# Kernel optimization log

Hardware: AMD Instinct MI355X
Metric: run time of the kernel (lower is better)

The kernel has to match this reference:

```python
import jax, jax.numpy as jnp
import numpy as np

IN_V, OUT_V, IN_E = 64, 64, 64
B, N, E = 2, 1024, 8192


def setup_inputs() -> dict:
    key = jax.random.key(0)
    ks = jax.random.split(key, 8)
    return {
        "H_v": jax.random.normal(ks[0], (B * N, IN_V), dtype=jnp.float32),
        "H_e": jax.random.normal(ks[1], (B * E, IN_E), dtype=jnp.float32),
        "adj_e": jax.random.uniform(ks[2], (B * E, E), dtype=jnp.float32),
        "adj_v": jax.random.uniform(ks[3], (B * N, N), dtype=jnp.float32),
        "T": jax.random.uniform(ks[4], (B * N, E), dtype=jnp.float32),
        "weight": jax.random.normal(ks[5], (IN_V, OUT_V), dtype=jnp.float32) * (1.0 / np.sqrt(OUT_V)),
        "p": jax.random.normal(ks[6], (1, IN_E), dtype=jnp.float32),
        "bias": jax.random.normal(ks[7], (OUT_V,), dtype=jnp.float32) * (1.0 / np.sqrt(OUT_V)),
    }


def reference(H_v, H_e, adj_e, adj_v, T, weight, p, bias):
    # node_layer=True branch of AlternateConvolution
    b = adj_v.shape[0] // adj_v.shape[1]
    n = adj_v.shape[1]
    e = adj_e.shape[1]
    H_v = H_v.reshape(b, n, -1)            # [B,N,in_v]
    H_e = H_e.reshape(b, e, -1)            # [B,E,in_e]
    adj_v = adj_v.reshape(b, n, n)         # [B,N,N]
    T = T.reshape(b, n, e)                 # [B,N,E]
    # diag_embed(H_e @ p^T) then T @ diag @ T^T == row-scale T by (H_e @ p^T) then GEMM
    scale = jnp.einsum('bef,f->be', H_e, p[0])                  # [B,E]
    multiplier1 = jnp.einsum('bne,be,bme->bnm', T, scale, T)    # [B,N,N]
    eye = jnp.eye(n, dtype=bool)
    M1 = jnp.where(eye[None, :, :], jnp.ones_like(multiplier1), multiplier1)
    adjusted_A = M1 * adj_v
    output = jnp.einsum('bnm,bmd->bnd', adjusted_A, H_v @ weight) + bias
    return output, H_e
```

## Files before the change

### kernel.cpp

```cpp
#include <hip/hip_runtime.h>

#define Bb 2
#define Nn 1024
#define Ee 8192
#define DV 64

typedef __attribute__((ext_vector_type(8))) short short8;
typedef __attribute__((ext_vector_type(8))) unsigned short ushort8;
typedef __attribute__((ext_vector_type(4))) float floatx4;

static __device__ __forceinline__ unsigned short f2bf(float f) {
    unsigned int u = __float_as_uint(f);
    unsigned int r = (u + 0x7FFFu + ((u >> 16) & 1u)) >> 16;
    return (unsigned short)r;
}
static __device__ __forceinline__ float bf2f(unsigned short u) {
    return __uint_as_float(((unsigned int)u) << 16);
}

__global__ __launch_bounds__(256) void scale_kernel(const float* __restrict__ He,
                                                    const float* __restrict__ p,
                                                    float* __restrict__ scale) {
    int wave = threadIdx.x >> 6;
    int lane = threadIdx.x & 63;
    int row = blockIdx.x * 4 + wave;
    float v = He[row * 64 + lane] * p[lane];
    #pragma unroll
    for (int off = 32; off > 0; off >>= 1) v += __shfl_xor(v, off);
    if (lane == 0) scale[row] = v;
}

__global__ __launch_bounds__(256) void cast_kernel(const float* __restrict__ T,
                                                   const float* __restrict__ scale,
                                                   unsigned short* __restrict__ Tsc,
                                                   unsigned short* __restrict__ Tpl) {
    size_t i4 = (size_t)blockIdx.x * 256 + threadIdx.x;
    size_t e0 = i4 * 4;
    int b = (int)(e0 >> 23);
    int e = (int)(e0 & 8191);
    floatx4 t = *(const floatx4*)&T[e0];
    floatx4 s = *(const floatx4*)&scale[(size_t)b * Ee + e];
    ushort4 sc, pl;
    sc.x = f2bf(t.x * s.x); sc.y = f2bf(t.y * s.y);
    sc.z = f2bf(t.z * s.z); sc.w = f2bf(t.w * s.w);
    pl.x = f2bf(t.x); pl.y = f2bf(t.y);
    pl.z = f2bf(t.z); pl.w = f2bf(t.w);
    *(ushort4*)&Tsc[e0] = sc;
    *(ushort4*)&Tpl[e0] = pl;
}

__global__ __launch_bounds__(256) void hw_kernel(const float* __restrict__ Hv,
                                                 const float* __restrict__ W,
                                                 float* __restrict__ HWo) {
    __shared__ float Ws[64 * 64];
    __shared__ float Hvs[4 * 64];
    int t = threadIdx.x;
    for (int i = t; i < 4096; i += 256) Ws[i] = W[i];
    int r0 = blockIdx.x * 4;
    Hvs[t] = Hv[(size_t)r0 * 64 + t];
    __syncthreads();
    int d = t & 63, rr = t >> 6;
    float acc = 0.f;
    #pragma unroll
    for (int c = 0; c < 64; ++c) acc += Hvs[rr * 64 + c] * Ws[c * 64 + d];
    HWo[(size_t)(r0 + rr) * 64 + d] = acc;
}

__global__ __launch_bounds__(256) void binit_kernel(const float* __restrict__ bias,
                                                    float* __restrict__ out) {
    int idx = (blockIdx.x * 256 + threadIdx.x) * 4;
    floatx4 bv = *(const floatx4*)&bias[idx & 63];
    *(floatx4*)&out[idx] = bv;
}

__global__ __launch_bounds__(256, 2) void mm_kernel(const unsigned short* __restrict__ Tsc,
                                                    const unsigned short* __restrict__ Tpl,
                                                    unsigned short* __restrict__ Ppart) {
    __shared__ __attribute__((aligned(16))) unsigned short As[128 * 64];
    __shared__ __attribute__((aligned(16))) unsigned short Bs[128 * 64];
    const int t = threadIdx.x;
    const int tile = blockIdx.x;
    const int b = blockIdx.y;
    const int s = blockIdx.z;

    int i = 0, rem = tile;
    while (rem >= 8 - i) { rem -= 8 - i; ++i; }
    const int j = i + rem;
    const int n0 = i * 128, m0 = j * 128;

    const int lane = t & 63;
    const int w = t >> 6;
    const int wr = w >> 1, wc = w & 1;
    const int quad = lane >> 4;
    const int l15 = lane & 15;
    const int l7 = l15 & 7;

    const int lr = lane >> 3;
    const int lc = (lane & 7) ^ lr;

    const int kc0 = (s * 128) / 7 * 64;
    const int kc1 = ((s + 1) * 128) / 7 * 64;

    const unsigned short* gA = Tsc + ((size_t)b * Nn + n0 + w * 32 + lr) * Ee + kc0 + lc * 8;
    const unsigned short* gB = Tpl + ((size_t)b * Nn + m0 + w * 32 + lr) * Ee + kc0 + lc * 8;
    unsigned short* lA = As + (w * 32) * 64 + lane * 8;
    unsigned short* lB = Bs + (w * 32) * 64 + lane * 8;

    floatx4 acc[4][4];
    #pragma unroll
    for (int a = 0; a < 4; ++a)
        #pragma unroll
        for (int c = 0; c < 4; ++c) acc[a][c] = (floatx4){0.f, 0.f, 0.f, 0.f};

    for (int k0 = kc0; k0 < kc1; k0 += 64) {
        #pragma unroll
        for (int u = 0; u < 4; ++u) {
            __builtin_amdgcn_global_load_lds(
                (const __attribute__((address_space(1))) unsigned int*)(gA + (size_t)u * 8 * Ee),
                (__attribute__((address_space(3))) unsigned int*)(lA + u * 8 * 64), 16, 0, 0);
            __builtin_amdgcn_global_load_lds(
                (const __attribute__((address_space(1))) unsigned int*)(gB + (size_t)u * 8 * Ee),
                (__attribute__((address_space(3))) unsigned int*)(lB + u * 8 * 64), 16, 0, 0);
        }
        gA += 64; gB += 64;
        __syncthreads();
        #pragma unroll
        for (int kk8 = 0; kk8 < 8; kk8 += 4) {
            short8 af[4], bf[4];
            #pragma unroll
            for (int a = 0; a < 4; ++a)
                af[a] = *(const short8*)&As[(wr * 64 + a * 16 + l15) * 64 + ((kk8 + quad) ^ l7) * 8];
            #pragma unroll
            for (int c = 0; c < 4; ++c)
                bf[c] = *(const short8*)&Bs[(wc * 64 + c * 16 + l15) * 64 + ((kk8 + quad) ^ l7) * 8];
            #pragma unroll
            for (int a = 0; a < 4; ++a)
                #pragma unroll
                for (int c = 0; c < 4; ++c)
                    acc[a][c] = __builtin_amdgcn_mfma_f32_16x16x32_bf16(af[a], bf[c], acc[a][c], 0, 0, 0);
        }
        __syncthreads();
    }

    unsigned short* P = Ppart + (((size_t)(b * 36 + tile)) * 7 + s) * 16384;
    #pragma unroll
    for (int a = 0; a < 4; ++a)
        #pragma unroll
        for (int c = 0; c < 4; ++c)
            #pragma unroll
            for (int v = 0; v < 4; ++v) {
                int r = wr * 64 + a * 16 + quad * 4 + v;
                int cc = wc * 64 + c * 16 + l15;
                P[r * 128 + cc] = f2bf(acc[a][c][v]);
            }
}

__global__ __launch_bounds__(256) void fuse_kernel(const unsigned short* __restrict__ Ppart,
                                                   const float* __restrict__ adj_v,
                                                   const float* __restrict__ HWo,
                                                   float* __restrict__ out) {
    __shared__ float Ls[64 * 68];
    __shared__ float Lsn[64 * 68];
    __shared__ float Lst[64 * 68];
    const int t = threadIdx.x;
    const int job = blockIdx.x;
    const int quad = blockIdx.y;
    const int b = job / 36;
    const int tile = job % 36;
    int i = 0, rem = tile;
    while (rem >= 8 - i) { rem -= 8 - i; ++i; }
    const int j = i + rem;
    const int qr = quad >> 1, qc = quad & 1;
    const int n0 = i * 128 + qr * 64;
    const int m0 = j * 128 + qc * 64;
    const unsigned short* P = Ppart + (size_t)job * 7 * 16384 + (qr * 64) * 128 + qc * 64;
    const float* AV = adj_v + (size_t)b * Nn * Nn;
    const float* HW = HWo + (size_t)b * Nn * 64;

    {
        int r = t >> 2, c0 = (t & 3) * 16;
        float sv[16];
        #pragma unroll
        for (int x = 0; x < 16; ++x) sv[x] = 0.f;
        #pragma unroll
        for (int sp = 0; sp < 7; ++sp) {
            const unsigned short* ps = P + sp * 16384 + r * 128 + c0;
            ushort8 u0 = *(const ushort8*)ps;
            ushort8 u1 = *(const ushort8*)(ps + 8);
            #pragma unroll
            for (int x = 0; x < 8; ++x) {
                sv[x] += bf2f(u0[x]);
                sv[8 + x] += bf2f(u1[x]);
            }
        }
        if (i == j && qr == qc) {
            int dcol = r - c0;
            if (dcol >= 0 && dcol < 16) sv[dcol] = 1.0f;
        }
        #pragma unroll
        for (int x4 = 0; x4 < 4; ++x4) {
            floatx4 v = (floatx4){sv[x4 * 4], sv[x4 * 4 + 1], sv[x4 * 4 + 2], sv[x4 * 4 + 3]};
            *(floatx4*)&Ls[r * 68 + c0 + x4 * 4] = v;
            floatx4 a = *(const floatx4*)&AV[(size_t)(n0 + r) * Nn + m0 + c0 + x4 * 4];
            floatx4 o = (floatx4){v.x * a.x, v.y * a.y, v.z * a.z, v.w * a.w};
            *(floatx4*)&Lsn[r * 68 + c0 + x4 * 4] = o;
        }
    }
    __syncthreads();
    if (i != j) {
        int m = t >> 2, r0 = (t & 3) * 16;
        #pragma unroll
        for (int x4 = 0; x4 < 4; ++x4) {
            floatx4 a = *(const floatx4*)&AV[(size_t)(m0 + m) * Nn + n0 + r0 + x4 * 4];
            floatx4 o;
            o.x = Ls[(r0 + x4 * 4 + 0) * 68 + m] * a.x;
            o.y = Ls[(r0 + x4 * 4 + 1) * 68 + m] * a.y;
            o.z = Ls[(r0 + x4 * 4 + 2) * 68 + m] * a.z;
            o.w = Ls[(r0 + x4 * 4 + 3) * 68 + m] * a.w;
            *(floatx4*)&Lst[m * 68 + r0 + x4 * 4] = o;
        }
    }
    __syncthreads();

    const int tr = t >> 4, tc = t & 15;
    {
        floatx4 acc[4];
        #pragma unroll
        for (int ii = 0; ii < 4; ++ii) acc[ii] = (floatx4){0.f, 0.f, 0.f, 0.f};
        #pragma unroll
        for (int k4 = 0; k4 < 64; k4 += 4) {
            floatx4 bmat[4];
            #pragma unroll
            for (int u = 0; u < 4; ++u)
                bmat[u] = *(const floatx4*)&HW[(size_t)(m0 + k4 + u) * 64 + tc * 4];
            #pragma unroll
            for (int ii = 0; ii < 4; ++ii) {
                floatx4 av = *(const floatx4*)&Lsn[(tr * 4 + ii) * 68 + k4];
                acc[ii] += av.x * bmat[0];
                acc[ii] += av.y * bmat[1];
                acc[ii] += av.z * bmat[2];
                acc[ii] += av.w * bmat[3];
            }
        }
        #pragma unroll
        for (int ii = 0; ii < 4; ++ii) {
            float* op = &out[(size_t)(b * Nn + n0 + tr * 4 + ii) * 64 + tc * 4];
            atomicAdd(op + 0, acc[ii].x);
            atomicAdd(op + 1, acc[ii].y);
            atomicAdd(op + 2, acc[ii].z);
            atomicAdd(op + 3, acc[ii].w);
        }
    }
    if (i != j) {
        floatx4 acc[4];
        #pragma unroll
        for (int ii = 0; ii < 4; ++ii) acc[ii] = (floatx4){0.f, 0.f, 0.f, 0.f};
        #pragma unroll
        for (int k4 = 0; k4 < 64; k4 += 4) {
            floatx4 bmat[4];
            #pragma unroll
            for (int u = 0; u < 4; ++u)
                bmat[u] = *(const floatx4*)&HW[(size_t)(n0 + k4 + u) * 64 + tc * 4];
            #pragma unroll
            for (int ii = 0; ii < 4; ++ii) {
                floatx4 av = *(const floatx4*)&Lst[(tr * 4 + ii) * 68 + k4];
                acc[ii] += av.x * bmat[0];
                acc[ii] += av.y * bmat[1];
                acc[ii] += av.z * bmat[2];
                acc[ii] += av.w * bmat[3];
            }
        }
        #pragma unroll
        for (int ii = 0; ii < 4; ++ii) {
            float* op = &out[(size_t)(b * Nn + m0 + tr * 4 + ii) * 64 + tc * 4];
            atomicAdd(op + 0, acc[ii].x);
            atomicAdd(op + 1, acc[ii].y);
            atomicAdd(op + 2, acc[ii].z);
            atomicAdd(op + 3, acc[ii].w);
        }
    }
}

extern "C" void kernel_launch(void* const* d_in, const int* in_sizes, int n_in,
                              void* d_out, int out_size, void* d_ws, size_t ws_size,
                              hipStream_t stream) {
    const float* H_v    = (const float*)d_in[0];
    const float* H_e    = (const float*)d_in[1];
    const float* adj_v  = (const float*)d_in[3];
    const float* T      = (const float*)d_in[4];
    const float* weight = (const float*)d_in[5];
    const float* p      = (const float*)d_in[6];
    const float* bias   = (const float*)d_in[7];
    float* out = (float*)d_out;

    char* ws = (char*)d_ws;
    float* scale          = (float*)ws;
    float* HWo            = (float*)(ws + (1 << 16));
    unsigned short* Tsc   = (unsigned short*)(ws + (1 << 20));
    unsigned short* Tpl   = (unsigned short*)(ws + (1 << 20) + (32u << 20));
    unsigned short* Ppart = (unsigned short*)(ws + (1 << 20) + (64u << 20));

    hipMemcpyAsync(out + (size_t)Bb * Nn * DV, H_e,
                   (size_t)Bb * Ee * 64 * sizeof(float),
                   hipMemcpyDeviceToDevice, stream);

    binit_kernel<<<dim3((Bb * Nn * DV) / 1024), dim3(256), 0, stream>>>(bias, out);
    scale_kernel<<<dim3(Bb * Ee / 4), dim3(256), 0, stream>>>(H_e, p, scale);
    cast_kernel<<<dim3((Bb * Nn * Ee / 4) / 256), dim3(256), 0, stream>>>(T, scale, Tsc, Tpl);
    hw_kernel<<<dim3(Bb * Nn / 4), dim3(256), 0, stream>>>(H_v, weight, HWo);
    mm_kernel<<<dim3(36, Bb, 7), dim3(256), 0, stream>>>(Tsc, Tpl, Ppart);
    fuse_kernel<<<dim3(36 * Bb, 4), dim3(256), 0, stream>>>(Ppart, adj_v, HWo, out);
}
```

Measured before the change: 711.3 us.

## Double-buffer LDS in mm_kernel and replace output atomics with partial-sum reduction

The bf16 MFMA GEMM kernel now uses two LDS buffers, so the async global-to-LDS load of the next K slice is issued before computing on the current one, with one barrier per iteration. The fuse kernel no longer uses per-element float atomicAdd into the output. It writes each 64-column contribution into a separate partial buffer indexed by source column block, and a new reduce kernel sums the 16 partials plus bias, which replaces the bias-init kernel. This trades atomic contention for extra workspace traffic and one more launch, and doubling LDS may limit occupancy.

```diff
diff --git a/kernel.cpp b/kernel.cpp
--- a/kernel.cpp
+++ b/kernel.cpp
@@ -66,18 +66,11 @@
     HWo[(size_t)(r0 + rr) * 64 + d] = acc;
 }
 
-__global__ __launch_bounds__(256) void binit_kernel(const float* __restrict__ bias,
-                                                    float* __restrict__ out) {
-    int idx = (blockIdx.x * 256 + threadIdx.x) * 4;
-    floatx4 bv = *(const floatx4*)&bias[idx & 63];
-    *(floatx4*)&out[idx] = bv;
-}
-
 __global__ __launch_bounds__(256, 2) void mm_kernel(const unsigned short* __restrict__ Tsc,
                                                     const unsigned short* __restrict__ Tpl,
                                                     unsigned short* __restrict__ Ppart) {
-    __shared__ __attribute__((aligned(16))) unsigned short As[128 * 64];
-    __shared__ __attribute__((aligned(16))) unsigned short Bs[128 * 64];
+    __shared__ __attribute__((aligned(16))) unsigned short As[2][128 * 64];
+    __shared__ __attribute__((aligned(16))) unsigned short Bs[2][128 * 64];
     const int t = threadIdx.x;
     const int tile = blockIdx.x;
     const int b = blockIdx.y;
@@ -100,11 +93,11 @@
 
     const int kc0 = (s * 128) / 7 * 64;
     const int kc1 = ((s + 1) * 128) / 7 * 64;
+    const int nIter = (kc1 - kc0) >> 6;
 
     const unsigned short* gA = Tsc + ((size_t)b * Nn + n0 + w * 32 + lr) * Ee + kc0 + lc * 8;
     const unsigned short* gB = Tpl + ((size_t)b * Nn + m0 + w * 32 + lr) * Ee + kc0 + lc * 8;
-    unsigned short* lA = As + (w * 32) * 64 + lane * 8;
-    unsigned short* lB = Bs + (w * 32) * 64 + lane * 8;
+    const int ldsOff = (w * 32) * 64 + lane * 8;
 
     floatx4 acc[4][4];
     #pragma unroll
@@ -112,7 +105,9 @@
         #pragma unroll
         for (int c = 0; c < 4; ++c) acc[a][c] = (floatx4){0.f, 0.f, 0.f, 0.f};
 
-    for (int k0 = kc0; k0 < kc1; k0 += 64) {
+    auto STAGE = [&](int buf) {
+        unsigned short* lA = &As[buf][0] + ldsOff;
+        unsigned short* lB = &Bs[buf][0] + ldsOff;
         #pragma unroll
         for (int u = 0; u < 4; ++u) {
             __builtin_amdgcn_global_load_lds(
@@ -123,16 +118,23 @@
                 (__attribute__((address_space(3))) unsigned int*)(lB + u * 8 * 64), 16, 0, 0);
         }
         gA += 64; gB += 64;
-        __syncthreads();
+    };
+
+    STAGE(0);
+    __syncthreads();
+    for (int it = 0; it < nIter; ++it) {
+        if (it + 1 < nIter) STAGE((it + 1) & 1);
+        const unsigned short* Ac = &As[it & 1][0];
+        const unsigned short* Bc = &Bs[it & 1][0];
         #pragma unroll
         for (int kk8 = 0; kk8 < 8; kk8 += 4) {
             short8 af[4], bf[4];
             #pragma unroll
             for (int a = 0; a < 4; ++a)
-                af[a] = *(const short8*)&As[(wr * 64 + a * 16 + l15) * 64 + ((kk8 + quad) ^ l7) * 8];
+                af[a] = *(const short8*)&Ac[(wr * 64 + a * 16 + l15) * 64 + ((kk8 + quad) ^ l7) * 8];
             #pragma unroll
             for (int c = 0; c < 4; ++c)
-                bf[c] = *(const short8*)&Bs[(wc * 64 + c * 16 + l15) * 64 + ((kk8 + quad) ^ l7) * 8];
+                bf[c] = *(const short8*)&Bc[(wc * 64 + c * 16 + l15) * 64 + ((kk8 + quad) ^ l7) * 8];
             #pragma unroll
             for (int a = 0; a < 4; ++a)
                 #pragma unroll
@@ -158,7 +160,7 @@
 __global__ __launch_bounds__(256) void fuse_kernel(const unsigned short* __restrict__ Ppart,
                                                    const float* __restrict__ adj_v,
                                                    const float* __restrict__ HWo,
-                                                   float* __restrict__ out) {
+                                                   float* __restrict__ parts) {
     __shared__ float Ls[64 * 68];
     __shared__ float Lsn[64 * 68];
     __shared__ float Lst[64 * 68];
@@ -242,14 +244,10 @@
                 acc[ii] += av.w * bmat[3];
             }
         }
-        #pragma unroll
-        for (int ii = 0; ii < 4; ++ii) {
-            float* op = &out[(size_t)(b * Nn + n0 + tr * 4 + ii) * 64 + tc * 4];
-            atomicAdd(op + 0, acc[ii].x);
-            atomicAdd(op + 1, acc[ii].y);
-            atomicAdd(op + 2, acc[ii].z);
-            atomicAdd(op + 3, acc[ii].w);
-        }
+        const size_t kbase = ((size_t)(j * 2 + qc) * (Bb * Nn) + (size_t)b * Nn + n0) * 64;
+        #pragma unroll
+        for (int ii = 0; ii < 4; ++ii)
+            *(floatx4*)&parts[kbase + (size_t)(tr * 4 + ii) * 64 + tc * 4] = acc[ii];
     }
     if (i != j) {
         floatx4 acc[4];
@@ -270,15 +268,22 @@
                 acc[ii] += av.w * bmat[3];
             }
         }
-        #pragma unroll
-        for (int ii = 0; ii < 4; ++ii) {
-            float* op = &out[(size_t)(b * Nn + m0 + tr * 4 + ii) * 64 + tc * 4];
-            atomicAdd(op + 0, acc[ii].x);
-            atomicAdd(op + 1, acc[ii].y);
-            atomicAdd(op + 2, acc[ii].z);
-            atomicAdd(op + 3, acc[ii].w);
-        }
-    }
+        const size_t kbase = ((size_t)(i * 2 + qr) * (Bb * Nn) + (size_t)b * Nn + m0) * 64;
+        #pragma unroll
+        for (int ii = 0; ii < 4; ++ii)
+            *(floatx4*)&parts[kbase + (size_t)(tr * 4 + ii) * 64 + tc * 4] = acc[ii];
+    }
+}
+
+__global__ __launch_bounds__(256) void reduce_kernel(const float* __restrict__ parts,
+                                                     const float* __restrict__ bias,
+                                                     float* __restrict__ out) {
+    size_t e0 = ((size_t)blockIdx.x * 256 + threadIdx.x) * 4;
+    floatx4 acc = *(const floatx4*)&bias[e0 & 63];
+    #pragma unroll
+    for (int k = 0; k < 16; ++k)
+        acc += *(const floatx4*)&parts[(size_t)k * (Bb * Nn * 64) + e0];
+    *(floatx4*)&out[e0] = acc;
 }
 
 extern "C" void kernel_launch(void* const* d_in, const int* in_sizes, int n_in,
@@ -299,15 +304,16 @@
     unsigned short* Tsc   = (unsigned short*)(ws + (1 << 20));
     unsigned short* Tpl   = (unsigned short*)(ws + (1 << 20) + (32u << 20));
     unsigned short* Ppart = (unsigned short*)(ws + (1 << 20) + (64u << 20));
+    float* parts          = (float*)(ws + (1 << 20) + (82u << 20));
 
     hipMemcpyAsync(out + (size_t)Bb * Nn * DV, H_e,
                    (size_t)Bb * Ee * 64 * sizeof(float),
                    hipMemcpyDeviceToDevice, stream);
 
-    binit_kernel<<<dim3((Bb * Nn * DV) / 1024), dim3(256), 0, stream>>>(bias, out);
     scale_kernel<<<dim3(Bb * Ee / 4), dim3(256), 0, stream>>>(H_e, p, scale);
     cast_kernel<<<dim3((Bb * Nn * Ee / 4) / 256), dim3(256), 0, stream>>>(T, scale, Tsc, Tpl);
     hw_kernel<<<dim3(Bb * Nn / 4), dim3(256), 0, stream>>>(H_v, weight, HWo);
     mm_kernel<<<dim3(36, Bb, 7), dim3(256), 0, stream>>>(Tsc, Tpl, Ppart);
-    fuse_kernel<<<dim3(36 * Bb, 4), dim3(256), 0, stream>>>(Ppart, adj_v, HWo, out);
-}
+    fuse_kernel<<<dim3(36 * Bb, 4), dim3(256), 0, stream>>>(Ppart, adj_v, HWo, parts);
+    reduce_kernel<<<dim3((Bb * Nn * 64 / 4) / 256), dim3(256), 0, stream>>>(parts, bias, out);
+}
```

Result: faster. 693.3 us (-2.5%).
